# Kernel optimization log

Hardware: AMD Instinct MI355X
Metric: run time of the kernel (lower is better)

## Reference

```python
import jax, jax.numpy as jnp
import numpy as np

B, T, HID = 1, 2048, 2048
H = 16            # num_heads == num_key_value_heads
D = HID // H      # head_dim == feature_dim == 128
EPS = 1e-5


def _layer_norm(x, eps=1e-5):
    mu = jnp.mean(x, axis=-1, keepdims=True)
    var = jnp.mean((x - mu) ** 2, axis=-1, keepdims=True)
    return (x - mu) * jax.lax.rsqrt(var + eps)


def _feature_map(x, gamma, beta):
    # ReBased feature map, flatten=False (parallel mode): affine then LayerNorm
    return _layer_norm(x * gamma + beta)


def setup_inputs() -> dict:
    key = jax.random.key(0)
    ks = jax.random.split(key, 8)
    s = HID ** -0.5
    return {
        "hidden_states": jax.random.normal(ks[0], (B, T, HID), jnp.float32),
        "Wq": jax.random.normal(ks[1], (HID, HID), jnp.float32) * s,
        "Wk": jax.random.normal(ks[2], (HID, HID), jnp.float32) * s,
        "Wv": jax.random.normal(ks[3], (HID, HID), jnp.float32) * s,
        "Wo": jax.random.normal(ks[4], (HID, HID), jnp.float32) * s,
        "gamma": 1.0 + 0.1 * jax.random.normal(ks[5], (D,), jnp.float32),
        "beta": 0.1 * jax.random.normal(ks[6], (D,), jnp.float32),
    }


def reference(hidden_states, Wq, Wk, Wv, Wo, gamma, beta):
    b, t, _ = hidden_states.shape
    # projections (nn.Linear: x @ W.T), split into heads: [b, t, h, d]
    q = (hidden_states @ Wq.T).reshape(b, t, H, D)
    k = (hidden_states @ Wk.T).reshape(b, t, H, D)
    v = (hidden_states @ Wv.T).reshape(b, t, H, D)
    # ReBased feature map (no quadratic flatten in parallel mode)
    q = _feature_map(q, gamma, beta)
    k = _feature_map(k, gamma, beta)
    # parallel_rebased: scale q, quadratic score, causal mask, normalize
    q = q * (D ** -0.5)
    attn = jnp.einsum('bqhd,bkhd->bhqk', q, k) ** 2  # (q.k)^2
    mask = jnp.tril(jnp.ones((t, t), dtype=bool))
    attn = jnp.where(mask, attn, 0.0)
    o = jnp.einsum('bhqk,bkhd->bqhd', attn, v)       # [b, t, h, d]
    z = jnp.sum(attn, axis=-1)                       # [b, h, t]
    o = o / (jnp.swapaxes(z, 1, 2)[..., None] + EPS)
    o = o.reshape(b, t, H * D)
    return o @ Wo.T
```

## Files before the change

### kernel.cpp

```cpp
#include <hip/hip_runtime.h>
#include <hip/hip_bf16.h>
#include <stdint.h>

typedef __bf16 bf16;
typedef __bf16 v8bf __attribute__((ext_vector_type(8)));
typedef float  v4f  __attribute__((ext_vector_type(4)));

#define TSEQ   2048
#define HIDDIM 2048
#define NHEAD  16
#define HDIM   128

__device__ __forceinline__ void async16(void* lds, const void* g)
{
    __builtin_amdgcn_global_load_lds(
        (__attribute__((address_space(1))) void*)(uintptr_t)g,
        (__attribute__((address_space(3))) void*)(unsigned int)(uintptr_t)lds,
        16, 0, 0);
}

__global__ __launch_bounds__(256) void conv5(const float* __restrict__ s0, bf16* __restrict__ d0,
                                             const float* __restrict__ s1, bf16* __restrict__ d1,
                                             const float* __restrict__ s2, bf16* __restrict__ d2,
                                             const float* __restrict__ s3, bf16* __restrict__ d3,
                                             const float* __restrict__ s4, bf16* __restrict__ d4)
{
    const float* src; bf16* dst;
    switch (blockIdx.y) {
        case 0: src = s0; dst = d0; break;
        case 1: src = s1; dst = d1; break;
        case 2: src = s2; dst = d2; break;
        case 3: src = s3; dst = d3; break;
        default: src = s4; dst = d4; break;
    }
    const size_t i = ((size_t)blockIdx.x * 256 + threadIdx.x) * 8;
    const float4 a = *(const float4*)(src + i);
    const float4 b = *(const float4*)(src + i + 4);
    v8bf o;
    o[0] = (bf16)a.x; o[1] = (bf16)a.y; o[2] = (bf16)a.z; o[3] = (bf16)a.w;
    o[4] = (bf16)b.x; o[5] = (bf16)b.y; o[6] = (bf16)b.z; o[7] = (bf16)b.w;
    *(v8bf*)(dst + i) = o;
}

template <typename CT>
__device__ __forceinline__ void gemm_body(const bf16* __restrict__ A,
                                          const bf16* __restrict__ B,
                                          CT* __restrict__ C,
                                          int m0, int n0, int K, int ldc)
{
    __shared__ __attribute__((aligned(16))) bf16 sA[128*32];
    __shared__ __attribute__((aligned(16))) bf16 sB[128*32];
    const int tid  = threadIdx.x;
    const int lane = tid & 63;
    const int w    = tid >> 6;
    const int wm   = w >> 1, wn = w & 1;
    const int quad = lane >> 4, lr = lane & 15;
    const int srow = lane >> 2;
    const int scol = (lane & 3) * 8;

    const bf16* gA0 = A + (size_t)(m0 + w*32 + srow) * K + scol;
    const bf16* gB0 = B + (size_t)(n0 + w*32 + srow) * K + scol;
    bf16* lA0 = &sA[w*1024];
    bf16* lB0 = &sB[w*1024];

    v4f acc[4][4] = {};

    for (int kt = 0; kt < K; kt += 32) {
        __syncthreads();
        async16(lA0,       gA0 + kt);
        async16(lA0 + 512, gA0 + (size_t)16*K + kt);
        async16(lB0,       gB0 + kt);
        async16(lB0 + 512, gB0 + (size_t)16*K + kt);
        __syncthreads();
        v8bf a[4], b[4];
#pragma unroll
        for (int i = 0; i < 4; ++i)
            a[i] = *(const v8bf*)&sA[(wm*64 + i*16 + lr)*32 + quad*8];
#pragma unroll
        for (int j = 0; j < 4; ++j)
            b[j] = *(const v8bf*)&sB[(wn*64 + j*16 + lr)*32 + quad*8];
#pragma unroll
        for (int i = 0; i < 4; ++i)
#pragma unroll
            for (int j = 0; j < 4; ++j)
                acc[i][j] = __builtin_amdgcn_mfma_f32_16x16x32_bf16(a[i], b[j], acc[i][j], 0, 0, 0);
    }

#pragma unroll
    for (int i = 0; i < 4; ++i) {
        const int row_b = m0 + wm*64 + i*16 + quad*4;
#pragma unroll
        for (int j = 0; j < 4; ++j) {
            const int col = n0 + wn*64 + j*16 + lr;
#pragma unroll
            for (int r = 0; r < 4; ++r)
                C[(size_t)(row_b + r)*ldc + col] = (CT)acc[i][j][r];
        }
    }
}

__global__ __launch_bounds__(256) void gemm_qkv(const bf16* __restrict__ A,
    const bf16* __restrict__ Wq, const bf16* __restrict__ Wk, const bf16* __restrict__ Wv,
    bf16* __restrict__ qb, bf16* __restrict__ kb, bf16* __restrict__ vb)
{
    const int which = blockIdx.x >> 4;
    const int n0 = (blockIdx.x & 15) * 128;
    const int m0 = blockIdx.y * 128;
    const bf16* B = (which == 0) ? Wq : (which == 1) ? Wk : Wv;
    bf16* C = (which == 0) ? qb : (which == 1) ? kb : vb;
    gemm_body<bf16>(A, B, C, m0, n0, HIDDIM, HIDDIM);
}

__global__ __launch_bounds__(256) void gemm_out(const bf16* __restrict__ A,
    const bf16* __restrict__ B, float* __restrict__ C)
{
    __shared__ __attribute__((aligned(16))) bf16 sA[128*32];
    __shared__ __attribute__((aligned(16))) bf16 sB[64*32];
    const int m0 = blockIdx.y * 128, n0 = blockIdx.x * 64;
    const int K = HIDDIM, ldc = HIDDIM;
    const int tid  = threadIdx.x;
    const int lane = tid & 63;
    const int w    = tid >> 6;
    const int wm   = w >> 1, wn = w & 1;
    const int quad = lane >> 4, lr = lane & 15;
    const int srow = lane >> 2;
    const int scol = (lane & 3) * 8;

    const bf16* gA0 = A + (size_t)(m0 + w*32 + srow) * K + scol;
    const bf16* gB0 = B + (size_t)(n0 + w*16 + srow) * K + scol;
    bf16* lA0 = &sA[w*1024];
    bf16* lB0 = &sB[w*512];

    v4f acc[4][2] = {};

    for (int kt = 0; kt < K; kt += 32) {
        __syncthreads();
        async16(lA0,       gA0 + kt);
        async16(lA0 + 512, gA0 + (size_t)16*K + kt);
        async16(lB0,       gB0 + kt);
        __syncthreads();
        v8bf a[4], b[2];
#pragma unroll
        for (int i = 0; i < 4; ++i)
            a[i] = *(const v8bf*)&sA[(wm*64 + i*16 + lr)*32 + quad*8];
#pragma unroll
        for (int j = 0; j < 2; ++j)
            b[j] = *(const v8bf*)&sB[(wn*32 + j*16 + lr)*32 + quad*8];
#pragma unroll
        for (int i = 0; i < 4; ++i)
#pragma unroll
            for (int j = 0; j < 2; ++j)
                acc[i][j] = __builtin_amdgcn_mfma_f32_16x16x32_bf16(a[i], b[j], acc[i][j], 0, 0, 0);
    }

#pragma unroll
    for (int i = 0; i < 4; ++i) {
        const int row_b = m0 + wm*64 + i*16 + quad*4;
#pragma unroll
        for (int j = 0; j < 2; ++j) {
            const int col = n0 + wn*32 + j*16 + lr;
#pragma unroll
            for (int r = 0; r < 4; ++r)
                C[(size_t)(row_b + r)*ldc + col] = acc[i][j][r];
        }
    }
}

__global__ __launch_bounds__(256) void fmap(bf16* __restrict__ qb, bf16* __restrict__ kb,
                                            const float* __restrict__ gamma,
                                            const float* __restrict__ beta)
{
    const int rid  = blockIdx.x * 4 + (threadIdx.x >> 6);
    const int lane = threadIdx.x & 63;
    bf16* base = (rid < TSEQ*NHEAD) ? (qb + (size_t)rid * HDIM)
                                    : (kb + (size_t)(rid - TSEQ*NHEAD) * HDIM);
    const float scale = (rid < TSEQ*NHEAD) ? 0.08838834764831845f : 1.0f;

    const bf16 x0b = base[lane*2], x1b = base[lane*2+1];
    const float g0 = gamma[lane*2], g1 = gamma[lane*2+1];
    const float b0 = beta[lane*2],  b1 = beta[lane*2+1];
    float x0 = (float)x0b*g0 + b0;
    float x1 = (float)x1b*g1 + b1;
    float s  = x0 + x1;
    float sq = x0*x0 + x1*x1;
#pragma unroll
    for (int off = 1; off < 64; off <<= 1) { s += __shfl_xor(s, off); sq += __shfl_xor(sq, off); }
    const float mu   = s * (1.0f/128.0f);
    float var        = sq * (1.0f/128.0f) - mu*mu;
    var = fmaxf(var, 0.0f);
    const float rstd = rsqrtf(var + 1e-5f);
    base[lane*2]   = (bf16)((x0 - mu) * rstd * scale);
    base[lane*2+1] = (bf16)((x1 - mu) * rstd * scale);
}

__global__ __launch_bounds__(256) void transpose2048(const bf16* __restrict__ src,
                                                     bf16* __restrict__ dst)
{
    __shared__ __attribute__((aligned(16))) bf16 tile[64][72];
    const int t0 = blockIdx.y * 64, c0 = blockIdx.x * 64;
    const int tid = threadIdx.x;
    const int r = tid >> 3;
    const int c = (tid & 7) * 8;
#pragma unroll
    for (int p = 0; p < 2; ++p) {
        const int rr = r + p*32;
        *(v8bf*)&tile[rr][c] = *(const v8bf*)(src + (size_t)(t0+rr)*HIDDIM + c0 + c);
    }
    __syncthreads();
#pragma unroll
    for (int p = 0; p < 2; ++p) {
        const int orow = r + p*32;
        v8bf o;
#pragma unroll
        for (int i = 0; i < 8; ++i) o[i] = tile[c + i][orow];
        *(v8bf*)(dst + (size_t)(c0+orow)*HIDDIM + t0 + c) = o;
    }
}

__global__ __launch_bounds__(512, 2) void attn(const bf16* __restrict__ qb,
                                               const bf16* __restrict__ kb,
                                               const bf16* __restrict__ vt,
                                               bf16* __restrict__ ob)
{
    __shared__ __attribute__((aligned(16))) bf16 sK[2*64*136];
    __shared__ __attribute__((aligned(16))) bf16 sV[2*128*72];
    __shared__ __attribute__((aligned(16))) bf16 sS[2*64*72];
    __shared__ __attribute__((aligned(16))) float sO[64*129];
    __shared__ __attribute__((aligned(16))) float sZ[64*17];

    const int h    = blockIdx.y;
    const int pr   = blockIdx.x;
    const int tid  = threadIdx.x, lane = tid & 63;
    const int w    = tid >> 6;
    const int g    = w >> 2;
    const int ww   = w & 3;
    const int quad = lane >> 4, lr = lane & 15;
    const int rs   = tid >> 4;
    const int cs   = (tid & 15) * 8;

#pragma unroll
    for (int ti = 0; ti < 2; ++ti) {
        const int tile = ti ? pr : (31 - pr);
        const int nch  = tile + 1;

        v8bf qa[4];
        {
            const bf16* q0 = qb + (size_t)(tile*64 + ww*16 + lr)*HIDDIM + h*HDIM + quad*8;
#pragma unroll
            for (int ks = 0; ks < 4; ++ks)
                qa[ks] = *(const v8bf*)(q0 + ks*32);
        }

        v4f  o[8] = {};
        float z[4] = {0.f, 0.f, 0.f, 0.f};

        v8bf curK[4], curV[4], nxtK[4], nxtV[4];
#pragma unroll
        for (int p = 0; p < 4; ++p) {
            curK[p] = *(const v8bf*)(kb + (size_t)(rs + p*32)*HIDDIM + h*HDIM + cs);
            curV[p] = *(const v8bf*)(vt + (size_t)(h*HDIM + rs + p*32)*HIDDIM + cs);
        }

        for (int ich = 0; ich < nch; ich += 2) {
            __syncthreads();
#pragma unroll
            for (int p = 0; p < 4; ++p) {
                const int r = rs + p*32;
                *(v8bf*)&sK[(r>>6)*8704 + (r&63)*136 + cs] = curK[p];
            }
#pragma unroll
            for (int p = 0; p < 4; ++p)
                *(v8bf*)&sV[(cs>>6)*9216 + (rs + p*32)*72 + (cs & 63)] = curV[p];

            if (ich + 2 < nch) {
                const int s1 = (ich + 2) * 64;
#pragma unroll
                for (int p = 0; p < 4; ++p) {
                    nxtK[p] = *(const v8bf*)(kb + (size_t)(s1 + rs + p*32)*HIDDIM + h*HDIM + cs);
                    nxtV[p] = *(const v8bf*)(vt + (size_t)(h*HDIM + rs + p*32)*HIDDIM + s1 + cs);
                }
            }
            __syncthreads();

            const int ch = ich + g;
            if (ch < nch) {
                const bf16* sKg = &sK[g*8704];
                const bf16* sVg = &sV[g*9216];
                bf16*       sSg = &sS[g*4608];
                const bool  diag = (ch == tile);
                const int   s0   = ch * 64;

                v8bf kbf[4][4];
#pragma unroll
                for (int nj = 0; nj < 4; ++nj)
#pragma unroll
                    for (int ks = 0; ks < 4; ++ks)
                        kbf[nj][ks] = *(const v8bf*)&sKg[(nj*16 + lr)*136 + ks*32 + quad*8];
                const int row_l = ww*16 + quad*4;
                const int qg    = tile*64 + row_l;
#pragma unroll
                for (int nj = 0; nj < 4; ++nj) {
                    v4f s4 = {0.f, 0.f, 0.f, 0.f};
#pragma unroll
                    for (int ks = 0; ks < 4; ++ks)
                        s4 = __builtin_amdgcn_mfma_f32_16x16x32_bf16(qa[ks], kbf[nj][ks], s4, 0, 0, 0);
                    const int col = nj*16 + lr;
                    const int sg  = s0 + col;
#pragma unroll
                    for (int r = 0; r < 4; ++r) {
                        float val = s4[r] * s4[r];
                        if (diag && (sg > qg + r)) val = 0.0f;
                        const bf16 vb16 = (bf16)val;
                        z[r] += (float)vb16;
                        sSg[(row_l + r)*72 + col] = vb16;
                    }
                }

#pragma unroll
                for (int ks = 0; ks < 2; ++ks) {
                    const v8bf sa = *(const v8bf*)&sSg[(ww*16 + lr)*72 + ks*32 + quad*8];
#pragma unroll
                    for (int nd = 0; nd < 8; ++nd) {
                        const v8bf vbf = *(const v8bf*)&sVg[(nd*16 + lr)*72 + ks*32 + quad*8];
                        o[nd] = __builtin_amdgcn_mfma_f32_16x16x32_bf16(sa, vbf, o[nd], 0, 0, 0);
                    }
                }
            }

            if (ich + 2 < nch) {
#pragma unroll
                for (int p = 0; p < 4; ++p) { curK[p] = nxtK[p]; curV[p] = nxtV[p]; }
            }
        }

        const int row_l = ww*16 + quad*4;
        __syncthreads();
        if (g == 1) {
#pragma unroll
            for (int nd = 0; nd < 8; ++nd)
#pragma unroll
                for (int r = 0; r < 4; ++r)
                    sO[(row_l + r)*129 + nd*16 + lr] = o[nd][r];
#pragma unroll
            for (int r = 0; r < 4; ++r)
                sZ[(row_l + r)*17 + lr] = z[r];
        }
        __syncthreads();
        if (g == 0) {
#pragma unroll
            for (int nd = 0; nd < 8; ++nd)
#pragma unroll
                for (int r = 0; r < 4; ++r)
                    o[nd][r] += sO[(row_l + r)*129 + nd*16 + lr];
#pragma unroll
            for (int r = 0; r < 4; ++r) {
                float zz = z[r] + sZ[(row_l + r)*17 + lr];
                zz += __shfl_xor(zz, 1); zz += __shfl_xor(zz, 2);
                zz += __shfl_xor(zz, 4); zz += __shfl_xor(zz, 8);
                z[r] = zz + 1e-5f;
            }
            const size_t rbase = (size_t)(tile*64 + row_l)*HIDDIM + h*HDIM;
#pragma unroll
            for (int nd = 0; nd < 8; ++nd) {
                const int col = nd*16 + lr;
#pragma unroll
                for (int r = 0; r < 4; ++r)
                    ob[rbase + (size_t)r*HIDDIM + col] = (bf16)(o[nd][r] / z[r]);
            }
        }
    }
}

extern "C" void kernel_launch(void* const* d_in, const int* in_sizes, int n_in,
                              void* d_out, int out_size, void* d_ws, size_t ws_size,
                              hipStream_t stream)
{
    const float* hs    = (const float*)d_in[0];
    const float* Wq    = (const float*)d_in[1];
    const float* Wk    = (const float*)d_in[2];
    const float* Wv    = (const float*)d_in[3];
    const float* Wo    = (const float*)d_in[4];
    const float* gamma = (const float*)d_in[5];
    const float* beta  = (const float*)d_in[6];
    float* outp = (float*)d_out;

    const size_t MAT = (size_t)TSEQ * HIDDIM;

    bf16* ws   = (bf16*)d_ws;
    bf16* hs_b = ws + 0*MAT;
    bf16* vt   = hs_b;
    bf16* Wv_b = ws + 1*MAT;
    bf16* Wo_b = ws + 2*MAT;
    bf16* qb   = ws + 3*MAT;
    bf16* kb   = ws + 4*MAT;
    bf16* vb   = ws + 5*MAT;
    bf16* ob   = vb;
    bf16* Wq_b = (bf16*)d_out;
    bf16* Wk_b = (bf16*)d_out + MAT;

    conv5<<<dim3(2048, 5), 256, 0, stream>>>(hs, hs_b, Wq, Wq_b, Wk, Wk_b, Wv, Wv_b, Wo, Wo_b);
    gemm_qkv<<<dim3(48, 16), 256, 0, stream>>>(hs_b, Wq_b, Wk_b, Wv_b, qb, kb, vb);
    fmap<<<dim3(2*TSEQ*NHEAD/4), 256, 0, stream>>>(qb, kb, gamma, beta);
    transpose2048<<<dim3(32, 32), 256, 0, stream>>>(vb, vt);
    attn<<<dim3(16, 16), 512, 0, stream>>>(qb, kb, vt, ob);
    gemm_out<<<dim3(32, 16), 256, 0, stream>>>(ob, Wo_b, outp);
}
```

Before: 281.6 us.

## Rewrite QKV GEMM as 256x256 tile, 8-wave, double-buffered pipelined kernel

Replaces the 128x128, 4-wave, K=32 single-buffered QKV projection GEMM with a 256x256-tile, 512-thread kernel. It uses K=64 stages, XOR-swizzled LDS layout and double buffering, and interleaves async global-to-LDS loads with MFMA quadrants under explicit barriers and s_setprio. The aim is to hide load latency, cut LDS bank conflicts and raise arithmetic intensity per tile. The cost is only 192 blocks, which may underfill the GPU's CUs, plus 128KB of LDS per block, which limits occupancy.

```diff
diff --git a/kernel.cpp b/kernel.cpp
--- a/kernel.cpp
+++ b/kernel.cpp
@@ -42,73 +42,115 @@
     *(v8bf*)(dst + i) = o;
 }
 
-template <typename CT>
-__device__ __forceinline__ void gemm_body(const bf16* __restrict__ A,
-                                          const bf16* __restrict__ B,
-                                          CT* __restrict__ C,
-                                          int m0, int n0, int K, int ldc)
-{
-    __shared__ __attribute__((aligned(16))) bf16 sA[128*32];
-    __shared__ __attribute__((aligned(16))) bf16 sB[128*32];
-    const int tid  = threadIdx.x;
-    const int lane = tid & 63;
-    const int w    = tid >> 6;
-    const int wm   = w >> 1, wn = w & 1;
-    const int quad = lane >> 4, lr = lane & 15;
-    const int srow = lane >> 2;
-    const int scol = (lane & 3) * 8;
-
-    const bf16* gA0 = A + (size_t)(m0 + w*32 + srow) * K + scol;
-    const bf16* gB0 = B + (size_t)(n0 + w*32 + srow) * K + scol;
-    bf16* lA0 = &sA[w*1024];
-    bf16* lB0 = &sB[w*1024];
-
-    v4f acc[4][4] = {};
-
-    for (int kt = 0; kt < K; kt += 32) {
-        __syncthreads();
-        async16(lA0,       gA0 + kt);
-        async16(lA0 + 512, gA0 + (size_t)16*K + kt);
-        async16(lB0,       gB0 + kt);
-        async16(lB0 + 512, gB0 + (size_t)16*K + kt);
-        __syncthreads();
-        v8bf a[4], b[4];
-#pragma unroll
-        for (int i = 0; i < 4; ++i)
-            a[i] = *(const v8bf*)&sA[(wm*64 + i*16 + lr)*32 + quad*8];
-#pragma unroll
-        for (int j = 0; j < 4; ++j)
-            b[j] = *(const v8bf*)&sB[(wn*64 + j*16 + lr)*32 + quad*8];
-#pragma unroll
-        for (int i = 0; i < 4; ++i)
-#pragma unroll
-            for (int j = 0; j < 4; ++j)
-                acc[i][j] = __builtin_amdgcn_mfma_f32_16x16x32_bf16(a[i], b[j], acc[i][j], 0, 0, 0);
-    }
-
-#pragma unroll
-    for (int i = 0; i < 4; ++i) {
-        const int row_b = m0 + wm*64 + i*16 + quad*4;
-#pragma unroll
-        for (int j = 0; j < 4; ++j) {
-            const int col = n0 + wn*64 + j*16 + lr;
-#pragma unroll
-            for (int r = 0; r < 4; ++r)
-                C[(size_t)(row_b + r)*ldc + col] = (CT)acc[i][j][r];
-        }
-    }
-}
-
-__global__ __launch_bounds__(256) void gemm_qkv(const bf16* __restrict__ A,
+
+#define PBAR() do { __builtin_amdgcn_sched_barrier(0); __builtin_amdgcn_s_barrier(); \
+                    __builtin_amdgcn_sched_barrier(0); } while (0)
+
+#define ST(shalf, ghalf) do { \
+    async16((shalf) + w*512,        (ghalf) + (size_t)(srow0)*2048); \
+    async16((shalf) + 4096 + w*512, (ghalf) + (size_t)(srow0 + 64)*2048); \
+} while (0)
+
+#define RD_A(buf, mh) do { _Pragma("unroll") \
+    for (int mi_ = 0; mi_ < 4; ++mi_) { \
+        const bf16* p_ = &sA[(buf)*16384 + (wm*128 + (mh)*64 + mi_*16 + lr)*64]; \
+        a[mi_][0] = *(const v8bf*)(p_ + c0); \
+        a[mi_][1] = *(const v8bf*)(p_ + c1); } } while (0)
+
+#define RD_B(buf, nh) do { _Pragma("unroll") \
+    for (int nj_ = 0; nj_ < 2; ++nj_) { \
+        const bf16* p_ = &sB[(buf)*16384 + (wn*64 + (nh)*32 + nj_*16 + lr)*64]; \
+        b[(nh)*2+nj_][0] = *(const v8bf*)(p_ + c0); \
+        b[(nh)*2+nj_][1] = *(const v8bf*)(p_ + c1); } } while (0)
+
+#define MQ(mh, nh) do { _Pragma("unroll") \
+    for (int mi_ = 0; mi_ < 4; ++mi_) { _Pragma("unroll") \
+        for (int nj_ = 0; nj_ < 2; ++nj_) { \
+            acc[(mh)*4+mi_][(nh)*2+nj_] = __builtin_amdgcn_mfma_f32_16x16x32_bf16( \
+                a[mi_][0], b[(nh)*2+nj_][0], acc[(mh)*4+mi_][(nh)*2+nj_], 0, 0, 0); \
+            acc[(mh)*4+mi_][(nh)*2+nj_] = __builtin_amdgcn_mfma_f32_16x16x32_bf16( \
+                a[mi_][1], b[(nh)*2+nj_][1], acc[(mh)*4+mi_][(nh)*2+nj_], 0, 0, 0); \
+        } } } while (0)
+
+__global__ __launch_bounds__(512, 2) void gemm_qkv8(const bf16* __restrict__ A,
     const bf16* __restrict__ Wq, const bf16* __restrict__ Wk, const bf16* __restrict__ Wv,
     bf16* __restrict__ qb, bf16* __restrict__ kb, bf16* __restrict__ vb)
 {
-    const int which = blockIdx.x >> 4;
-    const int n0 = (blockIdx.x & 15) * 128;
-    const int m0 = blockIdx.y * 128;
+    __shared__ __attribute__((aligned(16))) bf16 sA[2*16384];
+    __shared__ __attribute__((aligned(16))) bf16 sB[2*16384];
+    const int which = blockIdx.x >> 3;
+    const int n0 = (blockIdx.x & 7) * 256;
+    const int m0 = blockIdx.y * 256;
     const bf16* B = (which == 0) ? Wq : (which == 1) ? Wk : Wv;
     bf16* C = (which == 0) ? qb : (which == 1) ? kb : vb;
-    gemm_body<bf16>(A, B, C, m0, n0, HIDDIM, HIDDIM);
+
+    const int tid  = threadIdx.x, l = tid & 63, w = tid >> 6;
+    const int wm   = w >> 2, wn = w & 3;
+    const int quad = l >> 4, lr = l & 15;
+    const int srow0 = w*8 + (l>>3);
+    const int scol  = ((l & 7) ^ ((l >> 3) & 7)) * 8;
+    const int c0 = (( quad     ) ^ (lr & 7)) * 8;
+    const int c1 = ((quad + 4  ) ^ (lr & 7)) * 8;
+
+    const bf16* Ag = A + (size_t)m0 * 2048 + scol;
+    const bf16* Bg = B + (size_t)n0 * 2048 + scol;
+
+    v4f  acc[8][4] = {};
+    v8bf a[4][2], b[4][2];
+
+    ST(&sA[0],          Ag);
+    ST(&sA[8192],       Ag + (size_t)128*2048);
+    ST(&sB[0],          Bg);
+    ST(&sB[8192],       Bg + (size_t)128*2048);
+    ST(&sB[16384],      Bg + 64);
+    ST(&sB[16384+8192], Bg + (size_t)128*2048 + 64);
+    asm volatile("s_waitcnt vmcnt(4)" ::: "memory");
+    __builtin_amdgcn_s_barrier();
+    __builtin_amdgcn_sched_barrier(0);
+
+#pragma unroll 1
+    for (int it = 0; it < 16; ++it) {
+        const int k1 = it*128 + 64;
+        const int k2 = (it*128 + 128) & 2047;
+        const int k3 = (it*128 + 192) & 2047;
+
+        RD_A(0, 0); RD_B(0, 0);
+        ST(&sA[16384], Ag + k1);
+        PBAR(); __builtin_amdgcn_s_setprio(1); MQ(0, 0); __builtin_amdgcn_s_setprio(0); PBAR();
+        RD_B(0, 1);
+        ST(&sA[16384+8192], Ag + (size_t)128*2048 + k1);
+        PBAR(); __builtin_amdgcn_s_setprio(1); MQ(0, 1); __builtin_amdgcn_s_setprio(0); PBAR();
+        RD_A(0, 1);
+        ST(&sB[0], Bg + k2);
+        PBAR(); __builtin_amdgcn_s_setprio(1); MQ(1, 0); __builtin_amdgcn_s_setprio(0); PBAR();
+        ST(&sB[8192], Bg + (size_t)128*2048 + k2);
+        asm volatile("s_waitcnt vmcnt(4)" ::: "memory");
+        PBAR(); __builtin_amdgcn_s_setprio(1); MQ(1, 1); __builtin_amdgcn_s_setprio(0); PBAR();
+        RD_A(1, 0); RD_B(1, 0);
+        ST(&sA[0], Ag + k2);
+        PBAR(); __builtin_amdgcn_s_setprio(1); MQ(0, 0); __builtin_amdgcn_s_setprio(0); PBAR();
+        RD_B(1, 1);
+        ST(&sA[8192], Ag + (size_t)128*2048 + k2);
+        PBAR(); __builtin_amdgcn_s_setprio(1); MQ(0, 1); __builtin_amdgcn_s_setprio(0); PBAR();
+        RD_A(1, 1);
+        ST(&sB[16384], Bg + k3);
+        PBAR(); __builtin_amdgcn_s_setprio(1); MQ(1, 0); __builtin_amdgcn_s_setprio(0); PBAR();
+        ST(&sB[16384+8192], Bg + (size_t)128*2048 + k3);
+        asm volatile("s_waitcnt vmcnt(4)" ::: "memory");
+        PBAR(); __builtin_amdgcn_s_setprio(1); MQ(1, 1); __builtin_amdgcn_s_setprio(0); PBAR();
+    }
+
+#pragma unroll
+    for (int mi = 0; mi < 8; ++mi) {
+        const int row = m0 + wm*128 + (mi >> 2)*64 + (mi & 3)*16 + quad*4;
+#pragma unroll
+        for (int nj = 0; nj < 4; ++nj) {
+            const int col = n0 + wn*64 + (nj >> 1)*32 + (nj & 1)*16 + lr;
+#pragma unroll
+            for (int r = 0; r < 4; ++r)
+                C[(size_t)(row + r)*2048 + col] = (bf16)acc[mi][nj][r];
+        }
+    }
 }
 
 __global__ __launch_bounds__(256) void gemm_out(const bf16* __restrict__ A,
@@ -399,7 +441,7 @@
     bf16* Wk_b = (bf16*)d_out + MAT;
 
     conv5<<<dim3(2048, 5), 256, 0, stream>>>(hs, hs_b, Wq, Wq_b, Wk, Wk_b, Wv, Wv_b, Wo, Wo_b);
-    gemm_qkv<<<dim3(48, 16), 256, 0, stream>>>(hs_b, Wq_b, Wk_b, Wv_b, qb, kb, vb);
+    gemm_qkv8<<<dim3(24, 8), 512, 0, stream>>>(hs_b, Wq_b, Wk_b, Wv_b, qb, kb, vb);
     fmap<<<dim3(2*TSEQ*NHEAD/4), 256, 0, stream>>>(qb, kb, gamma, beta);
     transpose2048<<<dim3(32, 32), 256, 0, stream>>>(vb, vt);
     attn<<<dim3(16, 16), 512, 0, stream>>>(qb, kb, vt, ob);
```

Result: no change. 278.2 us (-1.2%).
